# Performance work log

Hardware: AMD Instinct MI355X
Metric: run time of the kernel (lower is better)

Reference implementation:

```python
import jax, jax.numpy as jnp
import numpy as np

NEG_SLOPE = 0.2


def _gat_attention(edge_index, feats, att_src, att_dst, num_nodes):
    # edge_index: [2, E] int; feats: [N, D]
    row, col = edge_index[0], edge_index[1]
    src_scores = feats @ att_src  # [N]
    dst_scores = feats @ att_dst  # [N]
    e = src_scores[row] + dst_scores[col]  # [E]
    e = jnp.where(e >= 0, e, NEG_SLOPE * e)  # leaky_relu(0.2)
    # segment softmax over edges grouped by row (stable)
    m = jax.ops.segment_max(e, row, num_segments=num_nodes)  # [N]
    ex = jnp.exp(e - m[row])
    denom = jax.ops.segment_sum(ex, row, num_segments=num_nodes)  # [N]
    alpha = ex / denom[row]  # [E]
    # SpMM: out[r] = sum_{edges e with row=r} alpha_e * feats[col_e]
    return jax.ops.segment_sum(alpha[:, None] * feats[col], row, num_segments=num_nodes)


def setup_inputs() -> dict:
    key = jax.random.key(0)
    ks = jax.random.split(key, 8)
    N, E = 100000, 1600000
    IN, H, OUT = 256, 128, 64
    x = jax.random.normal(ks[0], (N, IN), dtype=jnp.float32)
    edge_index = jax.random.randint(ks[1], (2, E), 0, N, dtype=jnp.int64)
    W1 = jax.random.normal(ks[2], (H, IN), dtype=jnp.float32) * (1.0 / np.sqrt(IN))
    W2 = jax.random.normal(ks[3], (OUT, H), dtype=jnp.float32) * (1.0 / np.sqrt(H))
    att_src1 = jax.random.normal(ks[4], (H,), dtype=jnp.float32) * 0.1
    att_dst1 = jax.random.normal(ks[5], (H,), dtype=jnp.float32) * 0.1
    att_src2 = jax.random.normal(ks[6], (OUT,), dtype=jnp.float32) * 0.1
    att_dst2 = jax.random.normal(ks[7], (OUT,), dtype=jnp.float32) * 0.1
    return {"x": x, "edge_index": edge_index, "W1": W1, "W2": W2,
            "att_src1": att_src1, "att_dst1": att_dst1,
            "att_src2": att_src2, "att_dst2": att_dst2, "num_nodes": N}


def reference(x, edge_index, W1, W2, att_src1, att_dst1, att_src2, att_dst2, num_nodes):
    h = x @ W1.T  # [N, H]
    h = jax.nn.elu(_gat_attention(edge_index, h, att_src1, att_dst1, num_nodes))
    h = h @ W2.T  # [N, OUT]
    return _gat_attention(edge_index, h, att_src2, att_dst2, num_nodes)
```

## Files before the change

kernel.cpp:

```cpp
#include <hip/hip_runtime.h>
#include <hip/hip_fp16.h>
#include <math.h>

#define NEG_SLOPE 0.2f
typedef unsigned int u32;
typedef unsigned short u16;
typedef _Float16 f16;
typedef __attribute__((ext_vector_type(8))) _Float16 f16x8;
typedef __attribute__((ext_vector_type(4))) float f32x4;

__device__ __forceinline__ float2 unpack_h2(u32 v) {
    return __half22float2(*(const __half2*)&v);
}

template <int K, int OUT>
__global__ void build_bswz(const float* __restrict__ W, f16* __restrict__ dst) {
    constexpr int NREP = OUT / 16;
    constexpr int TOT = (K / 32) * NREP * 512;
    int idx = blockIdx.x * 256 + threadIdx.x;
    if (idx >= TOT) return;
    int i = idx & 7;
    int lane = (idx >> 3) & 63;
    int fj = (idx >> 9) % NREP;
    int kb = (idx >> 9) / NREP;
    int o = fj * 16 + (lane & 15);
    int k = kb * 32 + (lane >> 4) * 8 + i;
    dst[idx] = (f16)W[(size_t)o * K + k];
}

template <int K, int OUT, bool ELU, bool F16IN>
__global__ __launch_bounds__(256) void gemm_mfma(
        const void* __restrict__ Ap, const f16* __restrict__ Bswz,
        const float* __restrict__ asrc, const float* __restrict__ adst,
        f16* __restrict__ H, float* __restrict__ s_out, float* __restrict__ d_out_,
        int N) {
    constexpr int BM = 64;
    constexpr int LDA = K + 8;
    constexpr int NREP = OUT / 16;
    constexpr int KB = K / 32;
    __shared__ f16 As[BM * LDA];
    const int t = threadIdx.x;
    const int w = t >> 6, lane = t & 63;
    const int r16 = lane & 15, g = lane >> 4;
    const int n0 = blockIdx.x * BM;

    constexpr int F4PR = K / 4;
#pragma unroll
    for (int it = 0; it < BM * F4PR / 256; ++it) {
        int q = t + 256 * it;
        int m = q / F4PR, c = q % F4PR;
        int gr = n0 + m;
        float vx = 0.f, vy = 0.f, vz = 0.f, vw = 0.f;
        if (gr < N) {
            if (F16IN) {
                const f16* Af = (const f16*)Ap;
                uint2 raw = *(const uint2*)&Af[(size_t)gr * K + 4 * c];
                float2 lo = unpack_h2(raw.x), hi = unpack_h2(raw.y);
                vx = lo.x; vy = lo.y; vz = hi.x; vw = hi.y;
            } else {
                float4 v = *(const float4*)&((const float*)Ap)[(size_t)gr * K + 4 * c];
                vx = v.x; vy = v.y; vz = v.z; vw = v.w;
            }
        }
        if (ELU) {
            vx = vx > 0.f ? vx : expm1f(vx);
            vy = vy > 0.f ? vy : expm1f(vy);
            vz = vz > 0.f ? vz : expm1f(vz);
            vw = vw > 0.f ? vw : expm1f(vw);
        }
        f16 tmp[4] = {(f16)vx, (f16)vy, (f16)vz, (f16)vw};
        *(uint2*)&As[m * LDA + 4 * c] = *(uint2*)tmp;
    }
    __syncthreads();

    f32x4 acc[NREP];
#pragma unroll
    for (int j = 0; j < NREP; ++j) acc[j] = (f32x4){0.f, 0.f, 0.f, 0.f};

#pragma unroll
    for (int kb = 0; kb < KB; ++kb) {
        f16x8 afr = *(const f16x8*)&As[(w * 16 + r16) * LDA + kb * 32 + 8 * g];
#pragma unroll
        for (int j = 0; j < NREP; ++j) {
            f16x8 bfr = *(const f16x8*)&Bswz[(((kb * NREP) + j) << 9) + (lane << 3)];
            acc[j] = __builtin_amdgcn_mfma_f32_16x16x32_f16(afr, bfr, acc[j], 0, 0, 0);
        }
    }

#pragma unroll
    for (int reg = 0; reg < 4; ++reg) {
        int m = n0 + w * 16 + g * 4 + reg;
        float vs = 0.f, vd = 0.f;
        if (m < N) {
#pragma unroll
            for (int j = 0; j < NREP; ++j) {
                float val = acc[j][reg];
                H[(size_t)m * OUT + j * 16 + r16] = (f16)val;
                vs = fmaf(val, asrc[j * 16 + r16], vs);
                vd = fmaf(val, adst[j * 16 + r16], vd);
            }
        }
#pragma unroll
        for (int off = 8; off >= 1; off >>= 1) {
            vs += __shfl_down(vs, off, 16);
            vd += __shfl_down(vd, off, 16);
        }
        if (r16 == 0 && m < N) {
            s_out[m] = vs;
            d_out_[m] = vd;
        }
    }
}

#define BKT_CAP 12288
__global__ __launch_bounds__(256) void bin_kernel(
        const int* __restrict__ row, const int* __restrict__ col,
        int* __restrict__ gcnt, uint2* __restrict__ staging, int E, int NB) {
    __shared__ int hist[256];
    __shared__ int scn[256];
    __shared__ int start[256];
    __shared__ int cursor[256];
    __shared__ int gbase[256];
    __shared__ uint2 binned[4096];
    const int t = threadIdx.x;
    const int base = blockIdx.x * 4096;
    const int cnt = min(4096, E - base);

    hist[t] = 0;
    __syncthreads();

    int myr[16], myc[16];
#pragma unroll
    for (int it = 0; it < 16; ++it) {
        int q = t + 256 * it;
        if (q < cnt) {
            myr[it] = row[base + q];
            myc[it] = col[base + q];
            atomicAdd(&hist[myr[it] >> 9], 1);
        }
    }
    __syncthreads();

    int v = hist[t];
    scn[t] = v;
    __syncthreads();
    for (int off = 1; off < 256; off <<= 1) {
        int x = (t >= off) ? scn[t - off] : 0;
        __syncthreads();
        scn[t] += x;
        __syncthreads();
    }
    start[t] = scn[t] - v;
    cursor[t] = scn[t] - v;
    __syncthreads();

#pragma unroll
    for (int it = 0; it < 16; ++it) {
        int q = t + 256 * it;
        if (q < cnt) {
            int b = myr[it] >> 9;
            int slot = atomicAdd(&cursor[b], 1);
            binned[slot] = make_uint2((u32)myr[it], (u32)myc[it]);
        }
    }
    __syncthreads();

    if (t < NB && hist[t] > 0) gbase[t] = atomicAdd(&gcnt[t], hist[t]);
    __syncthreads();

    for (int q = t; q < cnt; q += 256) {
        uint2 e = binned[q];
        int b = (int)(e.x >> 9);
        int pos = gbase[b] + (q - start[b]);
        staging[(size_t)b * BKT_CAP + pos] = e;
    }
}

__global__ __launch_bounds__(256) void scan_gcnt(const int* __restrict__ gcnt,
                                                 int* __restrict__ gbase, int NB) {
    __shared__ int s[256];
    const int t = threadIdx.x;
    int v = (t < NB) ? gcnt[t] : 0;
    s[t] = v;
    __syncthreads();
    for (int off = 1; off < 256; off <<= 1) {
        int x = (t >= off) ? s[t - off] : 0;
        __syncthreads();
        s[t] += x;
        __syncthreads();
    }
    gbase[t] = s[t] - v;
}

__global__ __launch_bounds__(256) void csr_scatter2(
        const uint2* __restrict__ staging, const int* __restrict__ gcnt,
        const int* __restrict__ gbase, int* __restrict__ rp, int* __restrict__ cs,
        int N) {
    __shared__ int cnt[512];
    __shared__ int exc[512];
    const int b = blockIdx.x;
    const int t = threadIdx.x;
    cnt[t] = 0;
    cnt[t + 256] = 0;
    __syncthreads();
    const int n = gcnt[b];
    const int base = gbase[b];
    const size_t sb = (size_t)b * BKT_CAP;

    for (int i = t; i < n; i += 256)
        atomicAdd(&cnt[staging[sb + i].x & 511], 1);
    __syncthreads();

    int v0 = cnt[t], v1 = cnt[t + 256];
    exc[t] = v0;
    exc[t + 256] = v1;
    __syncthreads();
    for (int off = 1; off < 512; off <<= 1) {
        int x0 = (t >= off) ? exc[t - off] : 0;
        int x1 = exc[t + 256 - off];
        __syncthreads();
        exc[t] += x0;
        exc[t + 256] += x1;
        __syncthreads();
    }
    int e0 = exc[t] - v0, e1 = exc[t + 256] - v1;
    int r0 = (b << 9) + t, r1 = (b << 9) + t + 256;
    if (r0 <= N) rp[r0] = base + e0;
    if (r1 <= N) rp[r1] = base + e1;
    exc[t] = e0;
    exc[t + 256] = e1;
    __syncthreads();

    for (int i = t; i < n; i += 256) {
        uint2 e = staging[sb + i];
        int p = base + atomicAdd(&exc[e.x & 511], 1);
        cs[p] = (int)e.y;
    }
}

template <int D, bool OUTF32>
__global__ __launch_bounds__(256) void gat_csr_f16(
        const int* __restrict__ rp, const int* __restrict__ cs,
        const float* __restrict__ s, const float* __restrict__ d,
        const u32* __restrict__ fp,
        void* __restrict__ outp, int N) {
    constexpr int G = D / 4;
    constexpr int NSUB = 64 / G;
    const int wid = threadIdx.x >> 6;
    const int lane = threadIdx.x & 63;
    const int li = lane & (G - 1);
    const int sub = lane / G;
    const int r = blockIdx.x * 4 + wid;
    if (r >= N) return;
    const int start = rp[r], end = rp[r + 1];
    const int len = end - start;
    const uint2* fp2 = (const uint2*)fp;

    float4 acc = make_float4(0.f, 0.f, 0.f, 0.f);

    if (len > 0 && len <= 64) {
        const float sr = s[r];
        int c_l = 0;
        float e_l = -INFINITY;
        if (lane < len) {
            c_l = cs[start + lane];
            float e = sr + d[c_l];
            e_l = (e >= 0.f) ? e : NEG_SLOPE * e;
        }
        float m = e_l;
#pragma unroll
        for (int off = 32; off >= 1; off >>= 1) m = fmaxf(m, __shfl_xor(m, off));
        float ex_l = (lane < len) ? __expf(e_l - m) : 0.f;
        float den = ex_l;
#pragma unroll
        for (int off = 32; off >= 1; off >>= 1) den += __shfl_xor(den, off);
        const float a_l = ex_l * (1.f / den);

        for (int j = 0; j < len; j += 2 * NSUB) {
            int i0 = j + sub, i1 = j + NSUB + sub;
            int c0 = __shfl(c_l, i0);
            int c1 = __shfl(c_l, i1);
            float a0 = __shfl(a_l, i0);
            float a1 = __shfl(a_l, i1);
            uint2 v0 = fp2[(size_t)c0 * G + li];
            uint2 v1 = fp2[(size_t)c1 * G + li];
            float2 p0 = unpack_h2(v0.x), q0 = unpack_h2(v0.y);
            acc.x = fmaf(a0, p0.x, acc.x);
            acc.y = fmaf(a0, p0.y, acc.y);
            acc.z = fmaf(a0, q0.x, acc.z);
            acc.w = fmaf(a0, q0.y, acc.w);
            float2 p1 = unpack_h2(v1.x), q1 = unpack_h2(v1.y);
            acc.x = fmaf(a1, p1.x, acc.x);
            acc.y = fmaf(a1, p1.y, acc.y);
            acc.z = fmaf(a1, q1.x, acc.z);
            acc.w = fmaf(a1, q1.y, acc.w);
        }
    } else if (len > 64) {
        const float sr = s[r];
        float m = -INFINITY;
        for (int j = start + lane; j < end; j += 64) {
            float e = sr + d[cs[j]];
            e = (e >= 0.f) ? e : NEG_SLOPE * e;
            m = fmaxf(m, e);
        }
#pragma unroll
        for (int off = 32; off >= 1; off >>= 1) m = fmaxf(m, __shfl_xor(m, off));
        float den = 0.f;
        for (int j = start + lane; j < end; j += 64) {
            float e = sr + d[cs[j]];
            e = (e >= 0.f) ? e : NEG_SLOPE * e;
            den += __expf(e - m);
        }
#pragma unroll
        for (int off = 32; off >= 1; off >>= 1) den += __shfl_xor(den, off);
        const float inv = 1.f / den;
        for (int j = start; j < end; ++j) {
            int c = __builtin_amdgcn_readfirstlane(cs[j]);
            float e = sr + d[c];
            e = (e >= 0.f) ? e : NEG_SLOPE * e;
            float alpha = __expf(e - m) * inv;
            if (sub == 0) {
                uint2 v = fp2[(size_t)c * G + li];
                float2 p = unpack_h2(v.x), q = unpack_h2(v.y);
                acc.x = fmaf(alpha, p.x, acc.x);
                acc.y = fmaf(alpha, p.y, acc.y);
                acc.z = fmaf(alpha, q.x, acc.z);
                acc.w = fmaf(alpha, q.y, acc.w);
            }
        }
    }

    if (NSUB == 4) {
        acc.x += __shfl_xor(acc.x, 16);
        acc.y += __shfl_xor(acc.y, 16);
        acc.z += __shfl_xor(acc.z, 16);
        acc.w += __shfl_xor(acc.w, 16);
    }
    if (NSUB >= 2) {
        acc.x += __shfl_xor(acc.x, 32);
        acc.y += __shfl_xor(acc.y, 32);
        acc.z += __shfl_xor(acc.z, 32);
        acc.w += __shfl_xor(acc.w, 32);
    }

    if (sub == 0) {
        if (OUTF32) {
            *(float4*)&((float*)outp)[(size_t)r * D + 4 * li] = acc;
        } else {
            __half2 h0 = __floats2half2_rn(acc.x, acc.y);
            __half2 h1 = __floats2half2_rn(acc.z, acc.w);
            uint2 pk = make_uint2(*(u32*)&h0, *(u32*)&h1);
            *(uint2*)&((f16*)outp)[(size_t)r * D + 4 * li] = pk;
        }
    }
}

extern "C" void kernel_launch(void* const* d_in, const int* in_sizes, int n_in,
                              void* d_out, int out_size, void* d_ws, size_t ws_size,
                              hipStream_t stream) {
    const float* x   = (const float*)d_in[0];
    const int*   edg = (const int*)d_in[1];
    const float* W1  = (const float*)d_in[2];
    const float* W2  = (const float*)d_in[3];
    const float* as1 = (const float*)d_in[4];
    const float* ad1 = (const float*)d_in[5];
    const float* as2 = (const float*)d_in[6];
    const float* ad2 = (const float*)d_in[7];

    const int N = in_sizes[0] / 256;
    const int E = in_sizes[1] / 2;
    const int* row = edg;
    const int* col = edg + E;
    const int NB = (N + 511) / 512;

    char* p = (char*)d_ws;
    f16* h1f = (f16*)p;     p += (size_t)N * 128 * 2;
    f16* h2f = (f16*)p;     p += (size_t)N * 64 * 2;
    char* g1s = p;
    f16* g1h = (f16*)g1s;
    uint2* staging = (uint2*)g1s;
    size_t g1_bytes = (size_t)N * 128 * 2;
    size_t stg_bytes = (size_t)NB * BKT_CAP * 8;
    p += (g1_bytes > stg_bytes) ? g1_bytes : stg_bytes;
    float* sm = (float*)p;  p += (size_t)N * 4 * 4;
    float* s1 = sm + (size_t)N * 0;
    float* d1 = sm + (size_t)N * 1;
    float* s2 = sm + (size_t)N * 2;
    float* d2 = sm + (size_t)N * 3;
    f16* B1 = (f16*)p;      p += (size_t)128 * 256 * 2;
    f16* B2 = (f16*)p;      p += (size_t)64 * 128 * 2;
    int* gcnt = (int*)p;    p += 256 * 4;
    int* gbase = (int*)p;   p += 256 * 4;
    int* rp  = (int*)p;     p += (size_t)(N + 1) * 4;
    int* cs  = (int*)p;     p += (size_t)E * 4;

    hipMemsetAsync(gcnt, 0, 256 * 4, stream);

    build_bswz<256, 128><<<128, 256, 0, stream>>>(W1, B1);
    build_bswz<128, 64><<<32, 256, 0, stream>>>(W2, B2);

    const int GB = (N + 63) / 64;

    bin_kernel<<<(E + 4095) / 4096, 256, 0, stream>>>(row, col, gcnt, staging, E, NB);
    scan_gcnt<<<1, 256, 0, stream>>>(gcnt, gbase, NB);
    csr_scatter2<<<NB, 256, 0, stream>>>(staging, gcnt, gbase, rp, cs, N);

    gemm_mfma<256, 128, false, false><<<GB, 256, 0, stream>>>(x, B1, as1, ad1, h1f, s1, d1, N);
    gat_csr_f16<128, false><<<(N + 3) / 4, 256, 0, stream>>>(rp, cs, s1, d1, (const u32*)h1f,
                                                             g1h, N);

    gemm_mfma<128, 64, true, true><<<GB, 256, 0, stream>>>(g1h, B2, as2, ad2, h2f, s2, d2, N);
    gat_csr_f16<64, true><<<(N + 3) / 4, 256, 0, stream>>>(rp, cs, s2, d2, (const u32*)h2f,
                                                           d_out, N);
}
```

Measured before the change: 221.5 us.

## Merge weight-swizzle launches, fold bucket scan into scatter, accumulate SpMM in half2

Combines the two weight-swizzle kernels into one launch and folds the bucket-count prefix scan into each csr_scatter2 block, so two kernel launches disappear. It also switches the short-row SpMM accumulation from fp32 FMAs to packed half2 FMAs, halving the arithmetic instructions per gathered element. The half-precision accumulation lowers numerical accuracy, and every scatter block now repeats the same 256-entry scan redundantly.

After: 218.5 us. No clear change (-1.3%).

```diff
diff --git a/kernel.cpp b/kernel.cpp
--- a/kernel.cpp
+++ b/kernel.cpp
@@ -13,19 +13,21 @@
     return __half22float2(*(const __half2*)&v);
 }
 
-template <int K, int OUT>
-__global__ void build_bswz(const float* __restrict__ W, f16* __restrict__ dst) {
-    constexpr int NREP = OUT / 16;
-    constexpr int TOT = (K / 32) * NREP * 512;
+__global__ void build_bswz_both(const float* __restrict__ W1, f16* __restrict__ B1,
+                                const float* __restrict__ W2, f16* __restrict__ B2) {
     int idx = blockIdx.x * 256 + threadIdx.x;
-    if (idx >= TOT) return;
-    int i = idx & 7;
-    int lane = (idx >> 3) & 63;
-    int fj = (idx >> 9) % NREP;
-    int kb = (idx >> 9) / NREP;
-    int o = fj * 16 + (lane & 15);
-    int k = kb * 32 + (lane >> 4) * 8 + i;
-    dst[idx] = (f16)W[(size_t)o * K + k];
+    if (idx < 32768) {
+        int i = idx & 7, lane = (idx >> 3) & 63, fj = (idx >> 9) & 7, kb = idx >> 12;
+        int o = fj * 16 + (lane & 15), k = kb * 32 + (lane >> 4) * 8 + i;
+        B1[idx] = (f16)W1[o * 256 + k];
+    } else {
+        int j = idx - 32768;
+        if (j < 8192) {
+            int i = j & 7, lane = (j >> 3) & 63, fj = (j >> 9) & 3, kb = j >> 11;
+            int o = fj * 16 + (lane & 15), k = kb * 32 + (lane >> 4) * 8 + i;
+            B2[j] = (f16)W2[o * 128 + k];
+        }
+    }
 }
 
 template <int K, int OUT, bool ELU, bool F16IN>
@@ -176,35 +178,28 @@
     }
 }
 
-__global__ __launch_bounds__(256) void scan_gcnt(const int* __restrict__ gcnt,
-                                                 int* __restrict__ gbase, int NB) {
-    __shared__ int s[256];
-    const int t = threadIdx.x;
-    int v = (t < NB) ? gcnt[t] : 0;
-    s[t] = v;
-    __syncthreads();
-    for (int off = 1; off < 256; off <<= 1) {
-        int x = (t >= off) ? s[t - off] : 0;
-        __syncthreads();
-        s[t] += x;
-        __syncthreads();
-    }
-    gbase[t] = s[t] - v;
-}
-
 __global__ __launch_bounds__(256) void csr_scatter2(
         const uint2* __restrict__ staging, const int* __restrict__ gcnt,
-        const int* __restrict__ gbase, int* __restrict__ rp, int* __restrict__ cs,
-        int N) {
+        int* __restrict__ rp, int* __restrict__ cs, int N) {
+    __shared__ int gsc[256];
     __shared__ int cnt[512];
     __shared__ int exc[512];
     const int b = blockIdx.x;
     const int t = threadIdx.x;
+
+    int gv = gcnt[t];
+    gsc[t] = gv;
     cnt[t] = 0;
     cnt[t + 256] = 0;
     __syncthreads();
+    for (int off = 1; off < 256; off <<= 1) {
+        int x = (t >= off) ? gsc[t - off] : 0;
+        __syncthreads();
+        gsc[t] += x;
+        __syncthreads();
+    }
     const int n = gcnt[b];
-    const int base = gbase[b];
+    const int base = gsc[b] - n;
     const size_t sb = (size_t)b * BKT_CAP;
 
     for (int i = t; i < n; i += 256)
@@ -276,6 +271,7 @@
         for (int off = 32; off >= 1; off >>= 1) den += __shfl_xor(den, off);
         const float a_l = ex_l * (1.f / den);
 
+        __half2 acch0 = __float2half2_rn(0.f), acch1 = acch0;
         for (int j = 0; j < len; j += 2 * NSUB) {
             int i0 = j + sub, i1 = j + NSUB + sub;
             int c0 = __shfl(c_l, i0);
@@ -284,17 +280,15 @@
             float a1 = __shfl(a_l, i1);
             uint2 v0 = fp2[(size_t)c0 * G + li];
             uint2 v1 = fp2[(size_t)c1 * G + li];
-            float2 p0 = unpack_h2(v0.x), q0 = unpack_h2(v0.y);
-            acc.x = fmaf(a0, p0.x, acc.x);
-            acc.y = fmaf(a0, p0.y, acc.y);
-            acc.z = fmaf(a0, q0.x, acc.z);
-            acc.w = fmaf(a0, q0.y, acc.w);
-            float2 p1 = unpack_h2(v1.x), q1 = unpack_h2(v1.y);
-            acc.x = fmaf(a1, p1.x, acc.x);
-            acc.y = fmaf(a1, p1.y, acc.y);
-            acc.z = fmaf(a1, q1.x, acc.z);
-            acc.w = fmaf(a1, q1.y, acc.w);
-        }
+            __half2 a02 = __half2half2(__float2half(a0));
+            __half2 a12 = __half2half2(__float2half(a1));
+            acch0 = __hfma2(a02, *(const __half2*)&v0.x, acch0);
+            acch1 = __hfma2(a02, *(const __half2*)&v0.y, acch1);
+            acch0 = __hfma2(a12, *(const __half2*)&v1.x, acch0);
+            acch1 = __hfma2(a12, *(const __half2*)&v1.y, acch1);
+        }
+        float2 lo = __half22float2(acch0), hi = __half22float2(acch1);
+        acc = make_float4(lo.x, lo.y, hi.x, hi.y);
     } else if (len > 64) {
         const float sr = s[r];
         float m = -INFINITY;
@@ -390,20 +384,17 @@
     f16* B1 = (f16*)p;      p += (size_t)128 * 256 * 2;
     f16* B2 = (f16*)p;      p += (size_t)64 * 128 * 2;
     int* gcnt = (int*)p;    p += 256 * 4;
-    int* gbase = (int*)p;   p += 256 * 4;
     int* rp  = (int*)p;     p += (size_t)(N + 1) * 4;
     int* cs  = (int*)p;     p += (size_t)E * 4;
 
     hipMemsetAsync(gcnt, 0, 256 * 4, stream);
 
-    build_bswz<256, 128><<<128, 256, 0, stream>>>(W1, B1);
-    build_bswz<128, 64><<<32, 256, 0, stream>>>(W2, B2);
+    build_bswz_both<<<160, 256, 0, stream>>>(W1, B1, W2, B2);
 
     const int GB = (N + 63) / 64;
 
     bin_kernel<<<(E + 4095) / 4096, 256, 0, stream>>>(row, col, gcnt, staging, E, NB);
-    scan_gcnt<<<1, 256, 0, stream>>>(gcnt, gbase, NB);
-    csr_scatter2<<<NB, 256, 0, stream>>>(staging, gcnt, gbase, rp, cs, N);
+    csr_scatter2<<<NB, 256, 0, stream>>>(staging, gcnt, rp, cs, N);
 
     gemm_mfma<256, 128, false, false><<<GB, 256, 0, stream>>>(x, B1, as1, ad1, h1f, s1, d1, N);
     gat_csr_f16<128, false><<<(N + 3) / 4, 256, 0, stream>>>(rp, cs, s1, d1, (const u32*)h1f,
```
